# Kernel optimization log

Measured on AMD Instinct MI355X. Metric: run time of the kernel, lower is better.

Reference implementation:

```python
import jax, jax.numpy as jnp
import numpy as np

EPS = 1e-8  # torch F.cosine_similarity default eps
NEG_INF = jnp.float32(-1e30)


def setup_inputs() -> dict:
    key = jax.random.key(0)
    k1, k2 = jax.random.split(key)
    N, M, D = 65536, 1024, 256
    embeddings = jax.random.normal(k1, (N, D), dtype=jnp.float32)
    prototypes = jax.random.normal(k2, (M, D), dtype=jnp.float32)
    counts = jnp.ones((M,), dtype=jnp.int64)  # all categories active
    return {"embeddings": embeddings, "prototypes": prototypes, "counts": counts}


def reference(embeddings, prototypes, counts):
    # Cosine similarity without materializing [N, M, D]:
    # sim[n, m] = <e_n, p_m> / max(||e_n|| * ||p_m||, eps)
    e_norm = jnp.linalg.norm(embeddings, axis=-1)            # [N]
    p_norm = jnp.linalg.norm(prototypes, axis=-1)            # [M]
    dots = jnp.einsum("nd,md->nm", embeddings, prototypes)   # [N, M]
    sim = dots / jnp.maximum(e_norm[:, None] * p_norm[None, :], EPS)
    # Mask inactive prototypes (counts == 0), matching `prototypes[active]`.
    active = counts > 0                                       # [M]
    sim = jnp.where(active[None, :], sim, NEG_INF)
    return jnp.argmax(sim, axis=-1)                           # [N] int
```

## Files before the change

### kernel.cpp

```cpp
#include <hip/hip_runtime.h>
#include <hip/hip_bf16.h>

typedef _Float16 f16x8 __attribute__((ext_vector_type(8)));
typedef float f32x4 __attribute__((ext_vector_type(4)));

#define TAU_Q 164
#define MASK_Q 2098790u

typedef const __attribute__((address_space(1))) void gas_void;
typedef __attribute__((address_space(3))) void las_void;

__device__ __forceinline__ void gload_lds16(const void* g, void* l) {
  __builtin_amdgcn_global_load_lds((gas_void*)g, (las_void*)l, 16, 0, 0);
}

__global__ __launch_bounds__(64) void prep_kernel(
    const float* __restrict__ P, const int* __restrict__ counts,
    float* __restrict__ q, int* __restrict__ wcount, f16x8* __restrict__ bhi) {
  const int m = blockIdx.x, lane = threadIdx.x;
  if (m == 0 && lane == 0) *wcount = 0;
  float4 v = *reinterpret_cast<const float4*>(P + (size_t)m * 256 + lane * 4);
  float s = v.x * v.x + v.y * v.y + v.z * v.z + v.w * v.w;
  for (int off = 32; off > 0; off >>= 1) s += __shfl_xor(s, off, 64);
  const float qm = (counts[m] > 0) ? (1.0f / sqrtf(s)) : 0.0f;
  if (lane == 0) q[m] = qm;
  if (lane < 32) {
    const int kg = lane;
    const float* src = P + (size_t)m * 256 + kg * 8;
    float4 v0 = *reinterpret_cast<const float4*>(src);
    float4 v1 = *reinterpret_cast<const float4*>(src + 4);
    float pe[8] = {v0.x, v0.y, v0.z, v0.w, v1.x, v1.y, v1.z, v1.w};
    f16x8 hi;
#pragma unroll
    for (int t = 0; t < 8; ++t) hi[t] = (_Float16)(pe[t] * qm);
    const int dst = ((m >> 4) * 8 + (kg >> 2)) * 64 + (kg & 3) * 16 + (m & 15);
    bhi[dst] = hi;
  }
}

__global__ __launch_bounds__(512) void screen_kernel(
    const float* __restrict__ E, const f16x8* __restrict__ bhi,
    int* __restrict__ out, int* __restrict__ wcount,
    int* __restrict__ wl, int wlcap) {
  __shared__ __align__(16) unsigned char ldsA[65536];
  __shared__ __align__(16) unsigned char ldsB[65536];

  const int tid = threadIdx.x;
  const int wave = tid >> 6, lane = tid & 63;
  const int rg = wave >> 2, cg = wave & 3;
  const int g = lane >> 4, c = lane & 15;
  const int blockRow = blockIdx.x * 128;
  const char* bhiB = (const char*)bhi;
  char* ldsBw = (char*)ldsB + wave * 8192;

  {
    const int row = tid >> 2, qq = tid & 3;
    const float* src = E + (size_t)(blockRow + row) * 256 + qq * 64;
    const int rswz = (row & 7) << 4;
#pragma unroll
    for (int o = 0; o < 8; ++o) {
      float4 v0 = *reinterpret_cast<const float4*>(src + o * 8);
      float4 v1 = *reinterpret_cast<const float4*>(src + o * 8 + 4);
      float e[8] = {v0.x, v0.y, v0.z, v0.w, v1.x, v1.y, v1.z, v1.w};
      f16x8 hi;
#pragma unroll
      for (int t = 0; t < 8; ++t) hi[t] = (_Float16)e[t];
      const int byte = (row * 512 + (qq * 64 + o * 8) * 2) ^ rswz;
      *reinterpret_cast<f16x8*>(ldsA + byte) = hi;
    }
  }

  auto stageB = [&](int b, int t) {
    const int ptn = t >> 3, kcn = t & 7;
    char* dstb = ldsBw + b * 4096;
#pragma unroll
    for (int fc = 0; fc < 4; ++fc) {
      const size_t src =
          (size_t)((((ptn * 16 + cg * 4 + fc) * 8 + kcn) << 10)) + (size_t)lane * 16;
      gload_lds16(bhiB + src, dstb + fc * 1024);
    }
  };

  stageB(0, 0);
  __syncthreads();

  unsigned t1[16], t2[16];
#pragma unroll
  for (int s = 0; s < 16; ++s) { t1[s] = 0u; t2[s] = 0u; }

#pragma unroll 1
  for (int pt = 0; pt < 4; ++pt) {
    f32x4 acc[4][4];
#pragma unroll
    for (int fr = 0; fr < 4; ++fr)
#pragma unroll
      for (int fc = 0; fc < 4; ++fc) acc[fr][fc] = (f32x4){0.f, 0.f, 0.f, 0.f};

#pragma unroll
    for (int kc = 0; kc < 8; ++kc) {
      const int t = pt * 8 + kc;
      const int buf = t & 1;

      if (t > 0) {
        asm volatile("s_waitcnt vmcnt(0)" ::: "memory");
        __builtin_amdgcn_sched_barrier(0);
      }
      f16x8 ah[4], bf[4];
#pragma unroll
      for (int fr = 0; fr < 4; ++fr) {
        const int rowA = rg * 64 + fr * 16 + c;
        const int ab = (rowA * 512 + kc * 64 + g * 16) ^ ((rowA & 7) << 4);
        ah[fr] = *reinterpret_cast<const f16x8*>(ldsA + ab);
      }
      {
        const char* bbase = ldsBw + buf * 4096 + (size_t)lane * 16;
#pragma unroll
        for (int fc = 0; fc < 4; ++fc)
          bf[fc] = *reinterpret_cast<const f16x8*>(bbase + fc * 1024);
      }
      if (t < 31) stageB(buf ^ 1, t + 1);
#pragma unroll
      for (int fr = 0; fr < 4; ++fr)
#pragma unroll
        for (int fc = 0; fc < 4; ++fc)
          acc[fr][fc] = __builtin_amdgcn_mfma_f32_16x16x32_f16(ah[fr], bf[fc], acc[fr][fc], 0, 0, 0);
    }

#pragma unroll
    for (int fc = 0; fc < 4; ++fc) {
      const unsigned mp = (unsigned)(1023 - (pt * 256 + cg * 64 + fc * 16 + c));
#pragma unroll
      for (int fr = 0; fr < 4; ++fr)
#pragma unroll
        for (int reg = 0; reg < 4; ++reg) {
          const int s = fr * 4 + reg;
          const float v = acc[fr][fc][reg];
          const unsigned k = ((unsigned)fmaf(v, 32768.0f, 2097152.0f) << 10) | mp;
          const unsigned lo = (k < t1[s]) ? k : t1[s];
          t1[s] = (k > t1[s]) ? k : t1[s];
          t2[s] = (lo > t2[s]) ? lo : t2[s];
        }
    }
  }

#pragma unroll
  for (int s = 0; s < 16; ++s) {
#pragma unroll
    for (int off = 1; off <= 8; off <<= 1) {
      const unsigned o1 = (unsigned)__shfl_xor((int)t1[s], off);
      const unsigned o2 = (unsigned)__shfl_xor((int)t2[s], off);
      const unsigned lo = (o1 < t1[s]) ? o1 : t1[s];
      t1[s] = (o1 > t1[s]) ? o1 : t1[s];
      const unsigned hi2 = (o2 > t2[s]) ? o2 : t2[s];
      t2[s] = (lo > hi2) ? lo : hi2;
    }
  }

  __syncthreads();
  unsigned* mg = reinterpret_cast<unsigned*>(ldsA);
  if (c == 0) {
#pragma unroll
    for (int s = 0; s < 16; ++s) {
      const int row = rg * 64 + (s >> 2) * 16 + g * 4 + (s & 3);
      mg[(row * 4 + cg) * 2 + 0] = t1[s];
      mg[(row * 4 + cg) * 2 + 1] = t2[s];
    }
  }
  __syncthreads();
  if (tid < 128) {
    unsigned T1 = mg[(tid * 4 + 0) * 2 + 0], T2 = mg[(tid * 4 + 0) * 2 + 1];
#pragma unroll
    for (int w = 1; w < 4; ++w) {
      const unsigned o1 = mg[(tid * 4 + w) * 2 + 0], o2 = mg[(tid * 4 + w) * 2 + 1];
      const unsigned lo = (o1 < T1) ? o1 : T1;
      T1 = (o1 > T1) ? o1 : T1;
      const unsigned hi2 = (o2 > T2) ? o2 : T2;
      T2 = (lo > hi2) ? lo : hi2;
    }
    const int grow = blockRow + tid;
    out[grow] = 1023 - (int)(T1 & 1023u);
    const unsigned iq1 = T1 >> 10, iq2 = T2 >> 10;
    if ((int)(iq1 - iq2) < TAU_Q || iq1 < MASK_Q) {
      const int p = atomicAdd(wcount, 1);
      if (p < wlcap) wl[p] = grow;
    }
  }
}

__global__ __launch_bounds__(256) void rescue_kernel(
    const float* __restrict__ E, const float* __restrict__ P,
    const float* __restrict__ q, int* __restrict__ out,
    const int* __restrict__ wcount, const int* __restrict__ wl, int wlcap) {
  __shared__ float Elds[16][260];
  __shared__ int rowsS[16];
  __shared__ float wv[16][4];
  __shared__ int wm[16][4];

  const int tid = threadIdx.x;
  const int wave = tid >> 6, lane = tid & 63;
  int total = *wcount;
  if (total > wlcap) total = wlcap;

  for (int b0 = blockIdx.x * 16; b0 < total; b0 += gridDim.x * 16) {
    const int nb = min(16, total - b0);
    __syncthreads();
    if (tid < 16) rowsS[tid] = wl[b0 + (tid < nb ? tid : 0)];
    __syncthreads();
#pragma unroll
    for (int u = 0; u < 4; ++u) {
      const int unit = u * 256 + tid, r = unit >> 6, k4 = unit & 63;
      *reinterpret_cast<float4*>(&Elds[r][k4 * 4]) =
          *reinterpret_cast<const float4*>(E + (size_t)rowsS[r] * 256 + k4 * 4);
    }
    __syncthreads();

    float acc[16][4];
#pragma unroll
    for (int r = 0; r < 16; ++r)
#pragma unroll
      for (int j = 0; j < 4; ++j) acc[r][j] = 0.f;

    for (int k16 = 0; k16 < 16; ++k16) {
#pragma unroll
      for (int jp = 0; jp < 2; ++jp) {
        float4 pv[2][4];
#pragma unroll
        for (int jj = 0; jj < 2; ++jj) {
          const float* ps = P + (size_t)(tid + 256 * (jp * 2 + jj)) * 256 + k16 * 16;
#pragma unroll
          for (int u = 0; u < 4; ++u)
            pv[jj][u] = *reinterpret_cast<const float4*>(ps + u * 4);
        }
#pragma unroll
        for (int r = 0; r < 16; ++r) {
#pragma unroll
          for (int jj = 0; jj < 2; ++jj) {
            const int j = jp * 2 + jj;
            float a = acc[r][j];
#pragma unroll
            for (int u = 0; u < 4; ++u) {
              const float4 ev = *reinterpret_cast<const float4*>(&Elds[r][k16 * 16 + u * 4]);
              a = fmaf(pv[jj][u].x, ev.x, a);
              a = fmaf(pv[jj][u].y, ev.y, a);
              a = fmaf(pv[jj][u].z, ev.z, a);
              a = fmaf(pv[jj][u].w, ev.w, a);
            }
            acc[r][j] = a;
          }
        }
      }
    }

    float qv[4];
#pragma unroll
    for (int j = 0; j < 4; ++j) qv[j] = q[tid + 256 * j];

#pragma unroll
    for (int r = 0; r < 16; ++r) {
      float bv = -3.0e38f;
      int bm = 0;
#pragma unroll
      for (int j = 0; j < 4; ++j) {
        const float v = (qv[j] > 0.f) ? acc[r][j] * qv[j] : -1.0e30f;
        if (v > bv) { bv = v; bm = tid + 256 * j; }
      }
#pragma unroll
      for (int off = 1; off <= 32; off <<= 1) {
        const float ov = __shfl_xor(bv, off);
        const int om = __shfl_xor(bm, off);
        if (ov > bv || (ov == bv && om < bm)) { bv = ov; bm = om; }
      }
      if (lane == 0) { wv[r][wave] = bv; wm[r][wave] = bm; }
    }
    __syncthreads();
    if (tid < 16) {
      float bv = wv[tid][0];
      int bm = wm[tid][0];
#pragma unroll
      for (int w = 1; w < 4; ++w) {
        const float ov = wv[tid][w];
        const int om = wm[tid][w];
        if (ov > bv || (ov == bv && om < bm)) { bv = ov; bm = om; }
      }
      if (tid < nb) out[rowsS[tid]] = bm;
    }
    __syncthreads();
  }
}

extern "C" void kernel_launch(void* const* d_in, const int* in_sizes, int n_in,
                              void* d_out, int out_size, void* d_ws, size_t ws_size,
                              hipStream_t stream) {
  const float* E = (const float*)d_in[0];
  const float* P = (const float*)d_in[1];
  const int* counts = (const int*)d_in[2];
  const int M = in_sizes[2];
  const int Dd = in_sizes[1] / M;
  const int N = in_sizes[0] / Dd;
  int* out = (int*)d_out;

  float* qv = (float*)d_ws;
  int* wcount = (int*)((char*)d_ws + 4096);
  f16x8* bhi = (f16x8*)((char*)d_ws + 8192);
  int* wl = (int*)((char*)d_ws + 8192 + 524288);
  long long cap = ((long long)ws_size - (8192 + 524288)) / 4;
  if (cap < 0) cap = 0;
  if (cap > N) cap = N;
  int wlcap = (int)cap;

  prep_kernel<<<M, 64, 0, stream>>>(P, counts, qv, wcount, bhi);
  screen_kernel<<<N / 128, 512, 0, stream>>>(E, bhi, out, wcount, wl, wlcap);
  rescue_kernel<<<256, 256, 0, stream>>>(E, P, qv, out, wcount, wl, wlcap);
}
```

Baseline: 121.6 us.

## Hold A fragments in registers and halve screen block to 256 threads

The screen kernel now loads its embedding rows straight from global memory into registers as fp16 MFMA fragments, replacing the staging of the A tile in a 64 KB LDS buffer. Blocks shrink to 4 waves arranged 2x2, and each wave sweeps 512 prototypes in 16 passes of 32 columns. LDS use drops from 128 KB to 16 KB, which should allow more resident blocks and cut LDS read traffic for A. In exchange each thread keeps 32 f16x8 registers for A, raising VGPR pressure, and the global reads of E are strided across lanes rather than coalesced.

```diff
diff --git a/kernel.cpp b/kernel.cpp
--- a/kernel.cpp
+++ b/kernel.cpp
@@ -38,97 +38,88 @@
   }
 }
 
-__global__ __launch_bounds__(512) void screen_kernel(
+__global__ __launch_bounds__(256) void screen_kernel(
     const float* __restrict__ E, const f16x8* __restrict__ bhi,
     int* __restrict__ out, int* __restrict__ wcount,
     int* __restrict__ wl, int wlcap) {
-  __shared__ __align__(16) unsigned char ldsA[65536];
-  __shared__ __align__(16) unsigned char ldsB[65536];
+  __shared__ __align__(16) unsigned char ldsB[16384];
 
   const int tid = threadIdx.x;
   const int wave = tid >> 6, lane = tid & 63;
-  const int rg = wave >> 2, cg = wave & 3;
+  const int rg = wave >> 1, cg = wave & 1;
   const int g = lane >> 4, c = lane & 15;
   const int blockRow = blockIdx.x * 128;
   const char* bhiB = (const char*)bhi;
-  char* ldsBw = (char*)ldsB + wave * 8192;
-
-  {
-    const int row = tid >> 2, qq = tid & 3;
-    const float* src = E + (size_t)(blockRow + row) * 256 + qq * 64;
-    const int rswz = (row & 7) << 4;
-#pragma unroll
-    for (int o = 0; o < 8; ++o) {
-      float4 v0 = *reinterpret_cast<const float4*>(src + o * 8);
-      float4 v1 = *reinterpret_cast<const float4*>(src + o * 8 + 4);
-      float e[8] = {v0.x, v0.y, v0.z, v0.w, v1.x, v1.y, v1.z, v1.w};
-      f16x8 hi;
-#pragma unroll
-      for (int t = 0; t < 8; ++t) hi[t] = (_Float16)e[t];
-      const int byte = (row * 512 + (qq * 64 + o * 8) * 2) ^ rswz;
-      *reinterpret_cast<f16x8*>(ldsA + byte) = hi;
-    }
-  }
+  char* ldsBw = (char*)ldsB + wave * 4096;
 
   auto stageB = [&](int b, int t) {
     const int ptn = t >> 3, kcn = t & 7;
-    char* dstb = ldsBw + b * 4096;
-#pragma unroll
-    for (int fc = 0; fc < 4; ++fc) {
-      const size_t src =
-          (size_t)((((ptn * 16 + cg * 4 + fc) * 8 + kcn) << 10)) + (size_t)lane * 16;
+    char* dstb = ldsBw + b * 2048;
+#pragma unroll
+    for (int fc = 0; fc < 2; ++fc) {
+      const int p16 = cg * 32 + ptn * 2 + fc;
+      const size_t src = (size_t)(((p16 * 8 + kcn) << 10)) + (size_t)lane * 16;
       gload_lds16(bhiB + src, dstb + fc * 1024);
     }
   };
 
   stageB(0, 0);
-  __syncthreads();
+
+  f16x8 a[4][8];
+#pragma unroll
+  for (int fr = 0; fr < 4; ++fr) {
+    const float* rowp = E + (size_t)(blockRow + rg * 64 + fr * 16 + c) * 256 + g * 8;
+#pragma unroll
+    for (int kc = 0; kc < 8; ++kc) {
+      const float* p = rowp + kc * 32;
+      float4 v0 = *reinterpret_cast<const float4*>(p);
+      float4 v1 = *reinterpret_cast<const float4*>(p + 4);
+      f16x8 h;
+      h[0] = (_Float16)v0.x; h[1] = (_Float16)v0.y;
+      h[2] = (_Float16)v0.z; h[3] = (_Float16)v0.w;
+      h[4] = (_Float16)v1.x; h[5] = (_Float16)v1.y;
+      h[6] = (_Float16)v1.z; h[7] = (_Float16)v1.w;
+      a[fr][kc] = h;
+    }
+  }
 
   unsigned t1[16], t2[16];
 #pragma unroll
   for (int s = 0; s < 16; ++s) { t1[s] = 0u; t2[s] = 0u; }
 
 #pragma unroll 1
-  for (int pt = 0; pt < 4; ++pt) {
-    f32x4 acc[4][4];
+  for (int pt = 0; pt < 16; ++pt) {
+    f32x4 acc[4][2];
 #pragma unroll
     for (int fr = 0; fr < 4; ++fr)
 #pragma unroll
-      for (int fc = 0; fc < 4; ++fc) acc[fr][fc] = (f32x4){0.f, 0.f, 0.f, 0.f};
+      for (int fc = 0; fc < 2; ++fc) acc[fr][fc] = (f32x4){0.f, 0.f, 0.f, 0.f};
 
 #pragma unroll
     for (int kc = 0; kc < 8; ++kc) {
       const int t = pt * 8 + kc;
       const int buf = t & 1;
 
-      if (t > 0) {
-        asm volatile("s_waitcnt vmcnt(0)" ::: "memory");
-        __builtin_amdgcn_sched_barrier(0);
-      }
-      f16x8 ah[4], bf[4];
-#pragma unroll
-      for (int fr = 0; fr < 4; ++fr) {
-        const int rowA = rg * 64 + fr * 16 + c;
-        const int ab = (rowA * 512 + kc * 64 + g * 16) ^ ((rowA & 7) << 4);
-        ah[fr] = *reinterpret_cast<const f16x8*>(ldsA + ab);
-      }
+      asm volatile("s_waitcnt vmcnt(0)" ::: "memory");
+      __builtin_amdgcn_sched_barrier(0);
+      f16x8 bf[2];
       {
-        const char* bbase = ldsBw + buf * 4096 + (size_t)lane * 16;
-#pragma unroll
-        for (int fc = 0; fc < 4; ++fc)
+        const char* bbase = ldsBw + buf * 2048 + (size_t)lane * 16;
+#pragma unroll
+        for (int fc = 0; fc < 2; ++fc)
           bf[fc] = *reinterpret_cast<const f16x8*>(bbase + fc * 1024);
       }
-      if (t < 31) stageB(buf ^ 1, t + 1);
+      if (t < 127) stageB(buf ^ 1, t + 1);
 #pragma unroll
       for (int fr = 0; fr < 4; ++fr)
 #pragma unroll
-        for (int fc = 0; fc < 4; ++fc)
-          acc[fr][fc] = __builtin_amdgcn_mfma_f32_16x16x32_f16(ah[fr], bf[fc], acc[fr][fc], 0, 0, 0);
-    }
-
-#pragma unroll
-    for (int fc = 0; fc < 4; ++fc) {
-      const unsigned mp = (unsigned)(1023 - (pt * 256 + cg * 64 + fc * 16 + c));
+        for (int fc = 0; fc < 2; ++fc)
+          acc[fr][fc] = __builtin_amdgcn_mfma_f32_16x16x32_f16(a[fr][kc], bf[fc], acc[fr][fc], 0, 0, 0);
+    }
+
+#pragma unroll
+    for (int fc = 0; fc < 2; ++fc) {
+      const unsigned mp = (unsigned)(1023 - (cg * 512 + pt * 32 + fc * 16 + c));
 #pragma unroll
       for (int fr = 0; fr < 4; ++fr)
 #pragma unroll
@@ -157,26 +148,23 @@
   }
 
   __syncthreads();
-  unsigned* mg = reinterpret_cast<unsigned*>(ldsA);
+  unsigned* mg = reinterpret_cast<unsigned*>(ldsB);
   if (c == 0) {
 #pragma unroll
     for (int s = 0; s < 16; ++s) {
       const int row = rg * 64 + (s >> 2) * 16 + g * 4 + (s & 3);
-      mg[(row * 4 + cg) * 2 + 0] = t1[s];
-      mg[(row * 4 + cg) * 2 + 1] = t2[s];
+      mg[(row * 2 + cg) * 2 + 0] = t1[s];
+      mg[(row * 2 + cg) * 2 + 1] = t2[s];
     }
   }
   __syncthreads();
   if (tid < 128) {
-    unsigned T1 = mg[(tid * 4 + 0) * 2 + 0], T2 = mg[(tid * 4 + 0) * 2 + 1];
-#pragma unroll
-    for (int w = 1; w < 4; ++w) {
-      const unsigned o1 = mg[(tid * 4 + w) * 2 + 0], o2 = mg[(tid * 4 + w) * 2 + 1];
-      const unsigned lo = (o1 < T1) ? o1 : T1;
-      T1 = (o1 > T1) ? o1 : T1;
-      const unsigned hi2 = (o2 > T2) ? o2 : T2;
-      T2 = (lo > hi2) ? lo : hi2;
-    }
+    const unsigned a1v = mg[(tid * 2 + 0) * 2 + 0], a2v = mg[(tid * 2 + 0) * 2 + 1];
+    const unsigned b1v = mg[(tid * 2 + 1) * 2 + 0], b2v = mg[(tid * 2 + 1) * 2 + 1];
+    const unsigned lo = (a1v < b1v) ? a1v : b1v;
+    const unsigned T1 = (a1v > b1v) ? a1v : b1v;
+    unsigned T2 = (a2v > b2v) ? a2v : b2v;
+    T2 = (lo > T2) ? lo : T2;
     const int grow = blockRow + tid;
     out[grow] = 1023 - (int)(T1 & 1023u);
     const unsigned iq1 = T1 >> 10, iq2 = T2 >> 10;
@@ -309,6 +297,6 @@
   int wlcap = (int)cap;
 
   prep_kernel<<<M, 64, 0, stream>>>(P, counts, qv, wcount, bhi);
-  screen_kernel<<<N / 128, 512, 0, stream>>>(E, bhi, out, wcount, wl, wlcap);
+  screen_kernel<<<N / 128, 256, 0, stream>>>(E, bhi, out, wcount, wl, wlcap);
   rescue_kernel<<<256, 256, 0, stream>>>(E, P, qv, out, wcount, wl, wlcap);
 }
```

Result: slower. 185.1 us (+52.2%).
